# Optimization experiments

Hardware: AMD Instinct MI355X
Metric: run time of the kernel (lower is better)

The kernel has to match this reference:

```python
import jax, jax.numpy as jnp
import numpy as np

BN_EPS = 1e-5


def sparsemax(z):
    # z: [B, D]; sparse projection onto the simplex along last axis.
    D = z.shape[-1]
    z_sorted = jnp.flip(jnp.sort(z, axis=-1), axis=-1)          # descending
    cs = jnp.cumsum(z_sorted, axis=-1)                           # cumulative sums
    k = jnp.arange(1, D + 1, dtype=z.dtype)                      # 1..D
    support = (1.0 + k * z_sorted) > cs                          # support condition
    k_star = jnp.sum(support, axis=-1, keepdims=True)            # support size, int
    cs_k = jnp.take_along_axis(cs, k_star - 1, axis=-1)
    tau = (cs_k - 1.0) / k_star.astype(z.dtype)                  # threshold
    return jnp.maximum(z - tau, 0.0)


def setup_inputs() -> dict:
    key = jax.random.key(0)
    k1, k2, k3 = jax.random.split(key, 3)
    B, D = 32768, 1024
    a = jax.random.normal(k1, (B, D), dtype=jnp.float32)
    p = jax.random.uniform(k2, (B, D), dtype=jnp.float32)        # prior scales in (0,1)
    W = jax.random.normal(k3, (D, D), dtype=jnp.float32) * (1.0 / np.sqrt(D))
    b = jnp.zeros((D,), dtype=jnp.float32)
    gamma = jnp.ones((D,), dtype=jnp.float32)
    beta = jnp.zeros((D,), dtype=jnp.float32)
    return {"a": a, "p": p, "W": W, "b": b, "gamma": gamma, "beta": beta}


def reference(a, p, W, b, gamma, beta):
    # Linear: a @ W^T + b  (torch nn.Linear convention)
    h = jnp.einsum("bd,ed->be", a, W) + b
    # BatchNorm1d (training mode: batch stats, biased variance)
    mean = jnp.mean(h, axis=0)
    var = jnp.mean(jnp.square(h - mean), axis=0)
    h = (h - mean) * jax.lax.rsqrt(var + BN_EPS) * gamma + beta
    # Prior scaling, then sparsemax -> attention mask
    mask = sparsemax(p * h)
    return mask
```

## Files before the change

### kernel.cpp

```cpp
#include <hip/hip_runtime.h>
#include <hip/hip_fp16.h>
#include <stdint.h>

typedef _Float16 f16x8 __attribute__((ext_vector_type(8)));
typedef _Float16 f16x2 __attribute__((ext_vector_type(2)));
typedef float f32x4 __attribute__((ext_vector_type(4)));

#define BM 128
#define BN 128
#define BK 64

__device__ __forceinline__ void async_copy16(const void* g, void* l) {
  __builtin_amdgcn_global_load_lds(
      (__attribute__((address_space(1))) void*)(g),
      (__attribute__((address_space(3))) void*)(l),
      16, 0, 0);
}

__global__ __launch_bounds__(256) void cvt_f32_f16(const float* __restrict__ in,
                                                   _Float16* __restrict__ out,
                                                   size_t n) {
  size_t i = ((size_t)blockIdx.x * 256 + threadIdx.x) * 8;
  if (i + 8 > n) return;
  float4 u = *(const float4*)(in + i);
  float4 v = *(const float4*)(in + i + 4);
  f16x8 h;
  h[0] = (_Float16)u.x; h[1] = (_Float16)u.y; h[2] = (_Float16)u.z; h[3] = (_Float16)u.w;
  h[4] = (_Float16)v.x; h[5] = (_Float16)v.y; h[6] = (_Float16)v.z; h[7] = (_Float16)v.w;
  *(f16x8*)(out + i) = h;
}

template <bool H16>
__global__ __launch_bounds__(256) void gemm_af32(const float* __restrict__ Af,
                                                 const _Float16* __restrict__ Wh,
                                                 const float* __restrict__ bias,
                                                 void* __restrict__ Hout,
                                                 float* __restrict__ psum,
                                                 float* __restrict__ psumsq,
                                                 int M, int N, int K) {
  __shared__ __attribute__((aligned(16))) float    lsA[BM * BK];
  __shared__ __attribute__((aligned(16))) _Float16 lsB[BN * BK];

  const int tid  = threadIdx.x;
  const int wave = tid >> 6;
  const int lane = tid & 63;
  const int wrow = (wave >> 1) * 64;
  const int wcol = (wave & 1) * 64;
  const int l16  = lane & 15;
  const int quad = lane >> 4;

  const int nx = gridDim.x;
  const int li = blockIdx.y * nx + blockIdx.x;
  const int xcd = li & 7;
  const int jj  = li >> 3;
  const int bnT = jj % nx;
  const int bmT = xcd + (jj / nx) * 8;
  const int bm = bmT * BM;
  const int bn = bnT * BN;

  f32x4 acc[4][4];
#pragma unroll
  for (int i = 0; i < 4; ++i)
#pragma unroll
    for (int j = 0; j < 4; ++j) acc[i][j] = (f32x4){0.f, 0.f, 0.f, 0.f};

  for (int k0 = 0; k0 < K; k0 += BK) {
#pragma unroll
    for (int i = 0; i < 4; ++i) {
      const int basechunk = i * 256 + wave * 64;
      const int g   = basechunk + lane;
      const int row = g >> 3;
      const int kc  = ((g & 7) ^ (row & 7)) << 3;
      async_copy16(Wh + (size_t)(bn + row) * K + k0 + kc, &lsB[basechunk * 8]);
    }
#pragma unroll
    for (int i = 0; i < 8; ++i) {
      const int basechunk = i * 256 + wave * 64;
      const int g   = basechunk + lane;
      const int row = g >> 4;
      const int cc  = (g & 15) ^ (row & 15);
      async_copy16(Af + (size_t)(bm + row) * K + k0 + cc * 4, &lsA[basechunk * 4]);
    }
    __syncthreads();

#pragma unroll
    for (int kk = 0; kk < BK; kk += 32) {
      f16x8 af[4], bf[4];
#pragma unroll
      for (int i = 0; i < 4; ++i) {
        const int r = wrow + i * 16 + l16;
        const int c0 = (kk >> 2) + quad * 2;
        f32x4 a0 = *(const f32x4*)&lsA[(r * 16 + (c0 ^ (r & 15))) * 4];
        f32x4 a1 = *(const f32x4*)&lsA[(r * 16 + ((c0 + 1) ^ (r & 15))) * 4];
        f16x8 h;
        h[0] = (_Float16)a0[0]; h[1] = (_Float16)a0[1];
        h[2] = (_Float16)a0[2]; h[3] = (_Float16)a0[3];
        h[4] = (_Float16)a1[0]; h[5] = (_Float16)a1[1];
        h[6] = (_Float16)a1[2]; h[7] = (_Float16)a1[3];
        af[i] = h;
      }
#pragma unroll
      for (int j = 0; j < 4; ++j) {
        const int r = wcol + j * 16 + l16;
        const int col = ((kk >> 3) + quad) ^ (l16 & 7);
        bf[j] = *(const f16x8*)&lsB[r * 64 + col * 8];
      }
#pragma unroll
      for (int i = 0; i < 4; ++i)
#pragma unroll
        for (int j = 0; j < 4; ++j)
          acc[i][j] = __builtin_amdgcn_mfma_f32_16x16x32_f16(af[i], bf[j], acc[i][j], 0, 0, 0);
    }
    __syncthreads();
  }

#pragma unroll
  for (int j = 0; j < 4; ++j) {
    const int c = bn + wcol + j * 16 + l16;
    const float bv = bias[c];
    float s = 0.f, s2 = 0.f;
#pragma unroll
    for (int i = 0; i < 4; ++i) {
      const int r = bm + wrow + i * 16 + quad * 4;
      f32x4 v = acc[i][j];
      const float v0 = v[0] + bv, v1 = v[1] + bv, v2 = v[2] + bv, v3 = v[3] + bv;
      s += v0 + v1 + v2 + v3;
      s2 += v0 * v0 + v1 * v1 + v2 * v2 + v3 * v3;
      if constexpr (H16) {
        f16x2* H2 = (f16x2*)Hout;
        const size_t d0 = (size_t)(r >> 1) * N + c;
        H2[d0]     = (f16x2){(_Float16)v0, (_Float16)v1};
        H2[d0 + N] = (f16x2){(_Float16)v2, (_Float16)v3};
      } else {
        float* Cp = (float*)Hout + (size_t)r * N + c;
        Cp[0] = v0; Cp[(size_t)N] = v1; Cp[2 * (size_t)N] = v2; Cp[3 * (size_t)N] = v3;
      }
    }
    s  += __shfl_xor(s, 16, 64);  s  += __shfl_xor(s, 32, 64);
    s2 += __shfl_xor(s2, 16, 64); s2 += __shfl_xor(s2, 32, 64);
    if (quad == 0) {
      const size_t slot = (size_t)(bmT * 2 + (wave >> 1)) * N + c;
      psum[slot] = s;
      psumsq[slot] = s2;
    }
  }
}

__global__ __launch_bounds__(256) void gemm_fallback(const float* __restrict__ Af,
                                                     const float* __restrict__ Wf,
                                                     const float* __restrict__ bias,
                                                     float* __restrict__ C,
                                                     float* __restrict__ sum,
                                                     float* __restrict__ sumsq,
                                                     int M, int N, int K) {
  __shared__ __attribute__((aligned(16))) _Float16 lsA[BM * BK];
  __shared__ __attribute__((aligned(16))) _Float16 lsB[BN * BK];
  const int tid  = threadIdx.x;
  const int wave = tid >> 6;
  const int lane = tid & 63;
  const int wrow = (wave >> 1) * 64;
  const int wcol = (wave & 1) * 64;
  const int l16  = lane & 15;
  const int quad = lane >> 4;
  const int bm = blockIdx.y * BM;
  const int bn = blockIdx.x * BN;

  f32x4 acc[4][4];
#pragma unroll
  for (int i = 0; i < 4; ++i)
#pragma unroll
    for (int j = 0; j < 4; ++j) acc[i][j] = (f32x4){0.f, 0.f, 0.f, 0.f};

  for (int k0 = 0; k0 < K; k0 += BK) {
#pragma unroll
    for (int i = 0; i < 4; ++i) {
      const int g   = i * 256 + tid;
      const int row = g >> 3;
      const int kc8 = g & 7;
      const int slot = row * 8 + (kc8 ^ (row & 7));
      {
        const float* src = Af + (size_t)(bm + row) * K + k0 + kc8 * 8;
        float4 u = *(const float4*)src;
        float4 v = *(const float4*)(src + 4);
        f16x8 h;
        h[0] = (_Float16)u.x; h[1] = (_Float16)u.y; h[2] = (_Float16)u.z; h[3] = (_Float16)u.w;
        h[4] = (_Float16)v.x; h[5] = (_Float16)v.y; h[6] = (_Float16)v.z; h[7] = (_Float16)v.w;
        *(f16x8*)&lsA[slot * 8] = h;
      }
      {
        const float* src = Wf + (size_t)(bn + row) * K + k0 + kc8 * 8;
        float4 u = *(const float4*)src;
        float4 v = *(const float4*)(src + 4);
        f16x8 h;
        h[0] = (_Float16)u.x; h[1] = (_Float16)u.y; h[2] = (_Float16)u.z; h[3] = (_Float16)u.w;
        h[4] = (_Float16)v.x; h[5] = (_Float16)v.y; h[6] = (_Float16)v.z; h[7] = (_Float16)v.w;
        *(f16x8*)&lsB[slot * 8] = h;
      }
    }
    __syncthreads();
#pragma unroll
    for (int kk = 0; kk < BK; kk += 32) {
      f16x8 af[4], bf[4];
#pragma unroll
      for (int i = 0; i < 4; ++i) {
        const int r = wrow + i * 16 + l16;
        const int col = ((kk >> 3) + quad) ^ (l16 & 7);
        af[i] = *(const f16x8*)&lsA[r * 64 + col * 8];
      }
#pragma unroll
      for (int j = 0; j < 4; ++j) {
        const int r = wcol + j * 16 + l16;
        const int col = ((kk >> 3) + quad) ^ (l16 & 7);
        bf[j] = *(const f16x8*)&lsB[r * 64 + col * 8];
      }
#pragma unroll
      for (int i = 0; i < 4; ++i)
#pragma unroll
        for (int j = 0; j < 4; ++j)
          acc[i][j] = __builtin_amdgcn_mfma_f32_16x16x32_f16(af[i], bf[j], acc[i][j], 0, 0, 0);
    }
    __syncthreads();
  }

#pragma unroll
  for (int j = 0; j < 4; ++j) {
    const int c = bn + wcol + j * 16 + l16;
    const float bv = bias[c];
    float s = 0.f, s2 = 0.f;
#pragma unroll
    for (int i = 0; i < 4; ++i) {
      const int r = bm + wrow + i * 16 + quad * 4;
      float* Cp = C + (size_t)r * N + c;
      f32x4 v = acc[i][j];
#pragma unroll
      for (int rr = 0; rr < 4; ++rr) {
        float val = v[rr] + bv;
        Cp[(size_t)rr * N] = val;
        s += val;
        s2 += val * val;
      }
    }
    s  += __shfl_xor(s, 16, 64);  s  += __shfl_xor(s, 32, 64);
    s2 += __shfl_xor(s2, 16, 64); s2 += __shfl_xor(s2, 32, 64);
    if (quad == 0) {
      atomicAdd(&sum[c], s);
      atomicAdd(&sumsq[c], s2);
    }
  }
}

__global__ __launch_bounds__(256) void bn_finalize_wave(const float* __restrict__ psum,
                                                        const float* __restrict__ psumsq,
                                                        const float* __restrict__ gamma,
                                                        const float* __restrict__ beta,
                                                        float* __restrict__ scale,
                                                        float* __restrict__ shift,
                                                        float invB, int S, int D) {
  const int wave = threadIdx.x >> 6;
  const int lane = threadIdx.x & 63;
  const int c = blockIdx.x * 4 + wave;
  float s = 0.f, q = 0.f;
  for (int u = lane; u < S; u += 64) {
    s += psum[(size_t)u * D + c];
    q += psumsq[(size_t)u * D + c];
  }
#pragma unroll
  for (int o = 32; o > 0; o >>= 1) {
    s += __shfl_xor(s, o, 64);
    q += __shfl_xor(q, o, 64);
  }
  if (lane == 0) {
    float mean = s * invB;
    float var  = q * invB - mean * mean;
    float rstd = rsqrtf(var + 1e-5f);
    float sc = rstd * gamma[c];
    scale[c] = sc;
    shift[c] = beta[c] - mean * sc;
  }
}

__global__ __launch_bounds__(256) void bn_finalize(const float* __restrict__ sum,
                                                   const float* __restrict__ sumsq,
                                                   const float* __restrict__ gamma,
                                                   const float* __restrict__ beta,
                                                   float* __restrict__ scale,
                                                   float* __restrict__ shift,
                                                   float invB) {
  const int c = blockIdx.x * 256 + threadIdx.x;
  float mean = sum[c] * invB;
  float var  = sumsq[c] * invB - mean * mean;
  float rstd = rsqrtf(var + 1e-5f);
  float sc = rstd * gamma[c];
  scale[c] = sc;
  shift[c] = beta[c] - mean * sc;
}

__global__ __launch_bounds__(256) void bn_sparsemax_h2(const _Float16* __restrict__ H2,
                                                       const float* __restrict__ P,
                                                       const float* __restrict__ scale,
                                                       const float* __restrict__ shift,
                                                       float* __restrict__ out, int D) {
  const int wave = threadIdx.x >> 6;
  const int lane = threadIdx.x & 63;
  const int row = blockIdx.x * 4 + wave;
  const int rp  = row >> 1;
  const int par = row & 1;

  const f16x8* Hc = (const f16x8*)(H2 + (size_t)rp * 2 * D);
  const f32x4* P4 = (const f32x4*)(P + (size_t)row * D);
  const f32x4* SC = (const f32x4*)scale;
  const f32x4* SH = (const f32x4*)shift;

  f32x4 z[4];
  float tot = 0.f;
#pragma unroll
  for (int j = 0; j < 4; ++j) {
    const int idx = j * 64 + lane;
    f16x8 h = Hc[idx];
    f32x4 hv = {(float)h[par], (float)h[2 + par], (float)h[4 + par], (float)h[6 + par]};
    f32x4 zz = P4[idx] * (hv * SC[idx] + SH[idx]);
    z[j] = zz;
    tot += zz[0] + zz[1] + zz[2] + zz[3];
  }
#pragma unroll
  for (int o = 32; o > 0; o >>= 1) tot += __shfl_xor(tot, o, 64);

  float tau = (tot - 1.0f) / (float)D;
  float kprev = -1.0f;
  for (int it = 0; it < 64; ++it) {
    float s = 0.f, kf = 0.f;
#pragma unroll
    for (int j = 0; j < 4; ++j)
#pragma unroll
      for (int c = 0; c < 4; ++c) {
        float zz = z[j][c];
        if (zz > tau) { s += zz; kf += 1.0f; }
      }
#pragma unroll
    for (int o = 32; o > 0; o >>= 1) {
      s  += __shfl_xor(s, o, 64);
      kf += __shfl_xor(kf, o, 64);
    }
    tau = (s - 1.0f) / kf;
    if (kf == kprev) break;
    kprev = kf;
  }

  f32x4* O4 = (f32x4*)(out + (size_t)row * D);
#pragma unroll
  for (int j = 0; j < 4; ++j) {
    const int idx = j * 64 + lane;
    f32x4 o;
#pragma unroll
    for (int c = 0; c < 4; ++c) o[c] = fmaxf(z[j][c] - tau, 0.f);
    O4[idx] = o;
  }
}

__global__ __launch_bounds__(256) void bn_sparsemax_f32(const float* __restrict__ H,
                                                        const float* __restrict__ P,
                                                        const float* __restrict__ scale,
                                                        const float* __restrict__ shift,
                                                        float* __restrict__ out, int D) {
  const int wave = threadIdx.x >> 6;
  const int lane = threadIdx.x & 63;
  const int row = blockIdx.x * 4 + wave;
  const size_t rowoff = (size_t)row * D;
  const f32x4* H4 = (const f32x4*)(H + rowoff);
  const f32x4* P4 = (const f32x4*)(P + rowoff);
  const f32x4* SC = (const f32x4*)scale;
  const f32x4* SH = (const f32x4*)shift;

  f32x4 z[4];
  float tot = 0.f;
#pragma unroll
  for (int j = 0; j < 4; ++j) {
    const int idx = j * 64 + lane;
    f32x4 zz = P4[idx] * (H4[idx] * SC[idx] + SH[idx]);
    z[j] = zz;
    tot += zz[0] + zz[1] + zz[2] + zz[3];
  }
#pragma unroll
  for (int o = 32; o > 0; o >>= 1) tot += __shfl_xor(tot, o, 64);

  float tau = (tot - 1.0f) / (float)D;
  float kprev = -1.0f;
  for (int it = 0; it < 64; ++it) {
    float s = 0.f, kf = 0.f;
#pragma unroll
    for (int j = 0; j < 4; ++j)
#pragma unroll
      for (int c = 0; c < 4; ++c) {
        float zz = z[j][c];
        if (zz > tau) { s += zz; kf += 1.0f; }
      }
#pragma unroll
    for (int o = 32; o > 0; o >>= 1) {
      s  += __shfl_xor(s, o, 64);
      kf += __shfl_xor(kf, o, 64);
    }
    tau = (s - 1.0f) / kf;
    if (kf == kprev) break;
    kprev = kf;
  }

  f32x4* O4 = (f32x4*)(out + rowoff);
#pragma unroll
  for (int j = 0; j < 4; ++j) {
    const int idx = j * 64 + lane;
    f32x4 o;
#pragma unroll
    for (int c = 0; c < 4; ++c) o[c] = fmaxf(z[j][c] - tau, 0.f);
    O4[idx] = o;
  }
}

extern "C" void kernel_launch(void* const* d_in, const int* in_sizes, int n_in,
                              void* d_out, int out_size, void* d_ws, size_t ws_size,
                              hipStream_t stream) {
  const float* a     = (const float*)d_in[0];
  const float* p     = (const float*)d_in[1];
  const float* W     = (const float*)d_in[2];
  const float* b     = (const float*)d_in[3];
  const float* gamma = (const float*)d_in[4];
  const float* beta  = (const float*)d_in[5];
  float* out = (float*)d_out;

  const int D = in_sizes[3];
  const int Brows = in_sizes[0] / D;
  const int K = D, N = D;
  const size_t na = (size_t)Brows * D;
  const size_t nw = (size_t)D * D;
  const int S = (Brows / BM) * 2;

  const size_t statsB = (size_t)D * S * sizeof(float);
  float* psum   = (float*)d_ws;
  float* psumsq = (float*)((char*)d_ws + statsB);
  float* wscale = (float*)((char*)d_ws + 2 * statsB);
  float* wshift = wscale + D;
  const size_t off_Wh = 2 * statsB + 16384;
  _Float16* Wh = (_Float16*)((char*)d_ws + off_Wh);
  _Float16* H2 = Wh + nw;
  const size_t need_h16 = off_Wh + (nw + na) * sizeof(_Float16);
  const size_t need_w   = off_Wh + nw * sizeof(_Float16);

  if (ws_size >= need_h16) {
    cvt_f32_f16<<<dim3((unsigned)(nw / 8 / 256)), 256, 0, stream>>>(W, Wh, nw);
    gemm_af32<true><<<dim3(N / BN, Brows / BM), 256, 0, stream>>>(
        a, Wh, b, H2, psum, psumsq, Brows, N, K);
    bn_finalize_wave<<<dim3(D / 4), 256, 0, stream>>>(psum, psumsq, gamma, beta,
                                                      wscale, wshift,
                                                      1.0f / (float)Brows, S, D);
    bn_sparsemax_h2<<<dim3(Brows / 4), 256, 0, stream>>>(H2, p, wscale, wshift, out, D);
  } else if (ws_size >= need_w) {
    cvt_f32_f16<<<dim3((unsigned)(nw / 8 / 256)), 256, 0, stream>>>(W, Wh, nw);
    gemm_af32<false><<<dim3(N / BN, Brows / BM), 256, 0, stream>>>(
        a, Wh, b, out, psum, psumsq, Brows, N, K);
    bn_finalize_wave<<<dim3(D / 4), 256, 0, stream>>>(psum, psumsq, gamma, beta,
                                                      wscale, wshift,
                                                      1.0f / (float)Brows, S, D);
    bn_sparsemax_f32<<<dim3(Brows / 4), 256, 0, stream>>>(out, p, wscale, wshift, out, D);
  } else {
    float* wsum   = (float*)d_ws;
    float* wsumsq = wsum + D;
    float* fscale = wsum + 2 * D;
    float* fshift = wsum + 3 * D;
    hipMemsetAsync(d_ws, 0, 2 * D * sizeof(float), stream);
    gemm_fallback<<<dim3(N / BN, Brows / BM), 256, 0, stream>>>(
        a, W, b, out, wsum, wsumsq, Brows, N, K);
    bn_finalize<<<dim3(D / 256), 256, 0, stream>>>(wsum, wsumsq, gamma, beta, fscale, fshift,
                                                   1.0f / (float)Brows);
    bn_sparsemax_f32<<<dim3(Brows / 4), 256, 0, stream>>>(out, p, fscale, fshift, out, D);
  }
}
```

Baseline: 414.0 us.

## Pre-convert activations to fp16 and use 256x256 four-stage pipelined GEMM

```diff
diff --git a/kernel.cpp b/kernel.cpp
--- a/kernel.cpp
+++ b/kernel.cpp
@@ -9,6 +9,10 @@
 #define BM 128
 #define BN 128
 #define BK 64
+
+#define GBM 256
+#define GBN 256
+#define GBK 32
 
 __device__ __forceinline__ void async_copy16(const void* g, void* l) {
   __builtin_amdgcn_global_load_lds(
@@ -19,128 +23,152 @@
 
 __global__ __launch_bounds__(256) void cvt_f32_f16(const float* __restrict__ in,
                                                    _Float16* __restrict__ out,
-                                                   size_t n) {
-  size_t i = ((size_t)blockIdx.x * 256 + threadIdx.x) * 8;
-  if (i + 8 > n) return;
-  float4 u = *(const float4*)(in + i);
-  float4 v = *(const float4*)(in + i + 4);
-  f16x8 h;
-  h[0] = (_Float16)u.x; h[1] = (_Float16)u.y; h[2] = (_Float16)u.z; h[3] = (_Float16)u.w;
-  h[4] = (_Float16)v.x; h[5] = (_Float16)v.y; h[6] = (_Float16)v.z; h[7] = (_Float16)v.w;
-  *(f16x8*)(out + i) = h;
-}
-
-template <bool H16>
-__global__ __launch_bounds__(256) void gemm_af32(const float* __restrict__ Af,
+                                                   size_t n8) {
+  const size_t stride = (size_t)gridDim.x * 256;
+  for (size_t i = (size_t)blockIdx.x * 256 + threadIdx.x; i < n8; i += stride) {
+    const float4* s = (const float4*)in + i * 2;
+    float4 u = s[0];
+    float4 v = s[1];
+    f16x8 h;
+    h[0] = (_Float16)u.x; h[1] = (_Float16)u.y; h[2] = (_Float16)u.z; h[3] = (_Float16)u.w;
+    h[4] = (_Float16)v.x; h[5] = (_Float16)v.y; h[6] = (_Float16)v.z; h[7] = (_Float16)v.w;
+    ((f16x8*)out)[i] = h;
+  }
+}
+
+__device__ __forceinline__ void stage32(const _Float16* __restrict__ src,
+                                        _Float16* __restrict__ dst,
+                                        int K, int wave, int lane) {
+#pragma unroll
+  for (int i = 0; i < 2; ++i) {
+    const int basechunk = i * 512 + wave * 64;
+    const int g   = basechunk + lane;
+    const int row = g >> 2;
+    const int sc  = (g & 3) ^ ((row >> 1) & 3);
+    async_copy16(src + (size_t)row * K + sc * 8, dst + basechunk * 8);
+  }
+}
+
+__global__ __launch_bounds__(512, 2) void gemm16(const _Float16* __restrict__ Ah,
                                                  const _Float16* __restrict__ Wh,
                                                  const float* __restrict__ bias,
-                                                 void* __restrict__ Hout,
+                                                 _Float16* __restrict__ Hout,
                                                  float* __restrict__ psum,
                                                  float* __restrict__ psumsq,
                                                  int M, int N, int K) {
-  __shared__ __attribute__((aligned(16))) float    lsA[BM * BK];
-  __shared__ __attribute__((aligned(16))) _Float16 lsB[BN * BK];
+  __shared__ __attribute__((aligned(16))) _Float16 lsA[4][GBM * GBK];
+  __shared__ __attribute__((aligned(16))) _Float16 lsB[4][GBN * GBK];
 
   const int tid  = threadIdx.x;
   const int wave = tid >> 6;
   const int lane = tid & 63;
-  const int wrow = (wave >> 1) * 64;
-  const int wcol = (wave & 1) * 64;
   const int l16  = lane & 15;
   const int quad = lane >> 4;
-
-  const int nx = gridDim.x;
-  const int li = blockIdx.y * nx + blockIdx.x;
+  const int wr   = wave >> 2;
+  const int wc   = wave & 3;
+
+  const int li  = blockIdx.x;
   const int xcd = li & 7;
   const int jj  = li >> 3;
-  const int bnT = jj % nx;
-  const int bmT = xcd + (jj / nx) * 8;
-  const int bm = bmT * BM;
-  const int bn = bnT * BN;
-
-  f32x4 acc[4][4];
-#pragma unroll
-  for (int i = 0; i < 4; ++i)
+  const int bnT = jj & 3;
+  const int bmT = xcd + (jj >> 2) * 8;
+  const int bm  = bmT * GBM;
+  const int bn  = bnT * GBN;
+
+  const _Float16* Ag = Ah + (size_t)bm * K;
+  const _Float16* Bg = Wh + (size_t)bn * K;
+
+  f32x4 acc[8][4];
+#pragma unroll
+  for (int i = 0; i < 8; ++i)
 #pragma unroll
     for (int j = 0; j < 4; ++j) acc[i][j] = (f32x4){0.f, 0.f, 0.f, 0.f};
 
-  for (int k0 = 0; k0 < K; k0 += BK) {
-#pragma unroll
-    for (int i = 0; i < 4; ++i) {
-      const int basechunk = i * 256 + wave * 64;
-      const int g   = basechunk + lane;
-      const int row = g >> 3;
-      const int kc  = ((g & 7) ^ (row & 7)) << 3;
-      async_copy16(Wh + (size_t)(bn + row) * K + k0 + kc, &lsB[basechunk * 8]);
-    }
-#pragma unroll
-    for (int i = 0; i < 8; ++i) {
-      const int basechunk = i * 256 + wave * 64;
-      const int g   = basechunk + lane;
-      const int row = g >> 4;
-      const int cc  = (g & 15) ^ (row & 15);
-      async_copy16(Af + (size_t)(bm + row) * K + k0 + cc * 4, &lsA[basechunk * 4]);
-    }
-    __syncthreads();
-
-#pragma unroll
-    for (int kk = 0; kk < BK; kk += 32) {
-      f16x8 af[4], bf[4];
-#pragma unroll
-      for (int i = 0; i < 4; ++i) {
-        const int r = wrow + i * 16 + l16;
-        const int c0 = (kk >> 2) + quad * 2;
-        f32x4 a0 = *(const f32x4*)&lsA[(r * 16 + (c0 ^ (r & 15))) * 4];
-        f32x4 a1 = *(const f32x4*)&lsA[(r * 16 + ((c0 + 1) ^ (r & 15))) * 4];
-        f16x8 h;
-        h[0] = (_Float16)a0[0]; h[1] = (_Float16)a0[1];
-        h[2] = (_Float16)a0[2]; h[3] = (_Float16)a0[3];
-        h[4] = (_Float16)a1[0]; h[5] = (_Float16)a1[1];
-        h[6] = (_Float16)a1[2]; h[7] = (_Float16)a1[3];
-        af[i] = h;
-      }
-#pragma unroll
-      for (int j = 0; j < 4; ++j) {
-        const int r = wcol + j * 16 + l16;
-        const int col = ((kk >> 3) + quad) ^ (l16 & 7);
-        bf[j] = *(const f16x8*)&lsB[r * 64 + col * 8];
-      }
-#pragma unroll
-      for (int i = 0; i < 4; ++i)
-#pragma unroll
-        for (int j = 0; j < 4; ++j)
-          acc[i][j] = __builtin_amdgcn_mfma_f32_16x16x32_f16(af[i], bf[j], acc[i][j], 0, 0, 0);
-    }
-    __syncthreads();
-  }
-
+  const int NT = K >> 5;
+
+#pragma unroll
+  for (int t = 0; t < 3; ++t) {
+    stage32(Ag + t * GBK, lsA[t], K, wave, lane);
+    stage32(Bg + t * GBK, lsB[t], K, wave, lane);
+  }
+  asm volatile("s_waitcnt vmcnt(8)" ::: "memory");
+  __builtin_amdgcn_s_barrier();
+  __builtin_amdgcn_sched_barrier(0);
+
+  const int pos   = quad ^ ((l16 >> 1) & 3);
+  const int abase = ((wr * 128 + l16) * 4 + pos) * 8;
+  const int bbase = ((wc * 64 + l16) * 4 + pos) * 8;
+
+#pragma unroll 1
+  for (int t = 0; t < NT; ++t) {
+    const _Float16* bufA = lsA[t & 3];
+    const _Float16* bufB = lsB[t & 3];
+    const int tp = t + 3;
+    const bool st = tp < NT;
+
+    if (st) stage32(Ag + (size_t)tp * GBK, lsA[tp & 3], K, wave, lane);
+    f16x8 bf[4], af[4];
+#pragma unroll
+    for (int j = 0; j < 4; ++j) bf[j] = *(const f16x8*)&bufB[bbase + j * 512];
+#pragma unroll
+    for (int i = 0; i < 4; ++i) af[i] = *(const f16x8*)&bufA[abase + i * 512];
+    __builtin_amdgcn_s_barrier();
+    asm volatile("s_waitcnt lgkmcnt(0)" ::: "memory");
+    __builtin_amdgcn_sched_barrier(0);
+    __builtin_amdgcn_s_setprio(1);
+#pragma unroll
+    for (int i = 0; i < 4; ++i)
+#pragma unroll
+      for (int j = 0; j < 4; ++j)
+        acc[i][j] = __builtin_amdgcn_mfma_f32_16x16x32_f16(af[i], bf[j], acc[i][j], 0, 0, 0);
+    __builtin_amdgcn_s_setprio(0);
+    __builtin_amdgcn_s_barrier();
+    __builtin_amdgcn_sched_barrier(0);
+
+    if (st) stage32(Bg + (size_t)tp * GBK, lsB[tp & 3], K, wave, lane);
+    f16x8 af2[4];
+#pragma unroll
+    for (int i = 0; i < 4; ++i) af2[i] = *(const f16x8*)&bufA[abase + (i + 4) * 512];
+    __builtin_amdgcn_s_barrier();
+    asm volatile("s_waitcnt lgkmcnt(0)" ::: "memory");
+    __builtin_amdgcn_sched_barrier(0);
+    __builtin_amdgcn_s_setprio(1);
+#pragma unroll
+    for (int i = 0; i < 4; ++i)
+#pragma unroll
+      for (int j = 0; j < 4; ++j)
+        acc[i + 4][j] = __builtin_amdgcn_mfma_f32_16x16x32_f16(af2[i], bf[j], acc[i + 4][j], 0, 0, 0);
+    __builtin_amdgcn_s_setprio(0);
+
+    if (t < NT - 3)       asm volatile("s_waitcnt vmcnt(8)" ::: "memory");
+    else if (t == NT - 3) asm volatile("s_waitcnt vmcnt(4)" ::: "memory");
+    else if (t == NT - 2) asm volatile("s_waitcnt vmcnt(0)" ::: "memory");
+    __builtin_amdgcn_s_barrier();
+    __builtin_amdgcn_sched_barrier(0);
+  }
+
+  f16x2* H2 = (f16x2*)Hout;
 #pragma unroll
   for (int j = 0; j < 4; ++j) {
-    const int c = bn + wcol + j * 16 + l16;
+    const int c = bn + wc * 64 + j * 16 + l16;
     const float bv = bias[c];
     float s = 0.f, s2 = 0.f;
 #pragma unroll
-    for (int i = 0; i < 4; ++i) {
-      const int r = bm + wrow + i * 16 + quad * 4;
+    for (int i = 0; i < 8; ++i) {
+      const int r = bm + wr * 128 + i * 16 + quad * 4;
       f32x4 v = acc[i][j];
       const float v0 = v[0] + bv, v1 = v[1] + bv, v2 = v[2] + bv, v3 = v[3] + bv;
-      s += v0 + v1 + v2 + v3;
+      s  += v0 + v1 + v2 + v3;
       s2 += v0 * v0 + v1 * v1 + v2 * v2 + v3 * v3;
-      if constexpr (H16) {
-        f16x2* H2 = (f16x2*)Hout;
-        const size_t d0 = (size_t)(r >> 1) * N + c;
-        H2[d0]     = (f16x2){(_Float16)v0, (_Float16)v1};
-        H2[d0 + N] = (f16x2){(_Float16)v2, (_Float16)v3};
-      } else {
-        float* Cp = (float*)Hout + (size_t)r * N + c;
-        Cp[0] = v0; Cp[(size_t)N] = v1; Cp[2 * (size_t)N] = v2; Cp[3 * (size_t)N] = v3;
-      }
+      const size_t d0 = (size_t)(r >> 1) * N + c;
+      H2[d0]     = (f16x2){(_Float16)v0, (_Float16)v1};
+      H2[d0 + N] = (f16x2){(_Float16)v2, (_Float16)v3};
     }
     s  += __shfl_xor(s, 16, 64);  s  += __shfl_xor(s, 32, 64);
     s2 += __shfl_xor(s2, 16, 64); s2 += __shfl_xor(s2, 32, 64);
     if (quad == 0) {
-      const size_t slot = (size_t)(bmT * 2 + (wave >> 1)) * N + c;
-      psum[slot] = s;
+      const size_t slot = (size_t)(bmT * 2 + wr) * N + c;
+      psum[slot]   = s;
       psumsq[slot] = s2;
     }
   }
@@ -431,7 +459,7 @@
   const int K = D, N = D;
   const size_t na = (size_t)Brows * D;
   const size_t nw = (size_t)D * D;
-  const int S = (Brows / BM) * 2;
+  const int S = (Brows / GBM) * 2;
 
   const size_t statsB = (size_t)D * S * sizeof(float);
   float* psum   = (float*)d_ws;
@@ -441,25 +469,22 @@
   const size_t off_Wh = 2 * statsB + 16384;
   _Float16* Wh = (_Float16*)((char*)d_ws + off_Wh);
   _Float16* H2 = Wh + nw;
-  const size_t need_h16 = off_Wh + (nw + na) * sizeof(_Float16);
-  const size_t need_w   = off_Wh + nw * sizeof(_Float16);
-
-  if (ws_size >= need_h16) {
-    cvt_f32_f16<<<dim3((unsigned)(nw / 8 / 256)), 256, 0, stream>>>(W, Wh, nw);
-    gemm_af32<true><<<dim3(N / BN, Brows / BM), 256, 0, stream>>>(
-        a, Wh, b, H2, psum, psumsq, Brows, N, K);
+  const size_t need = off_Wh + (nw + na) * sizeof(_Float16);
+  _Float16* Ah = (_Float16*)d_out;
+
+  const bool shape_ok = (Brows % GBM) == 0 && ((Brows / GBM) % 8) == 0 &&
+                        (N / GBN) == 4 && (N % GBN) == 0 &&
+                        (K % GBK) == 0 && (K / GBK) >= 4;
+
+  if (ws_size >= need && (size_t)out_size >= na * sizeof(_Float16) && shape_ok) {
+    cvt_f32_f16<<<dim3(512), 256, 0, stream>>>(W, Wh, nw / 8);
+    cvt_f32_f16<<<dim3(2048), 256, 0, stream>>>(a, Ah, na / 8);
+    gemm16<<<dim3((Brows / GBM) * (N / GBN)), 512, 0, stream>>>(
+        Ah, Wh, b, H2, psum, psumsq, Brows, N, K);
     bn_finalize_wave<<<dim3(D / 4), 256, 0, stream>>>(psum, psumsq, gamma, beta,
                                                       wscale, wshift,
                                                       1.0f / (float)Brows, S, D);
     bn_sparsemax_h2<<<dim3(Brows / 4), 256, 0, stream>>>(H2, p, wscale, wshift, out, D);
-  } else if (ws_size >= need_w) {
-    cvt_f32_f16<<<dim3((unsigned)(nw / 8 / 256)), 256, 0, stream>>>(W, Wh, nw);
-    gemm_af32<false><<<dim3(N / BN, Brows / BM), 256, 0, stream>>>(
-        a, Wh, b, out, psum, psumsq, Brows, N, K);
-    bn_finalize_wave<<<dim3(D / 4), 256, 0, stream>>>(psum, psumsq, gamma, beta,
-                                                      wscale, wshift,
-                                                      1.0f / (float)Brows, S, D);
-    bn_sparsemax_f32<<<dim3(Brows / 4), 256, 0, stream>>>(out, p, wscale, wshift, out, D);
   } else {
     float* wsum   = (float*)d_ws;
     float* wsumsq = wsum + D;
```

Result: slower. 515.1 us (+24.4%).
